# Optimization experiments

Hardware: AMD Instinct MI355X
Metric: run time of the kernel (lower is better)

## Reference

```python
import jax, jax.numpy as jnp
import numpy as np

B, H, S, D = 4, 16, 2048, 64


def setup_inputs() -> dict:
    key = jax.random.key(0)
    kq, kk, kv = jax.random.split(key, 3)
    q = jax.random.normal(kq, (B, H, S, D), dtype=jnp.float32)
    k = jax.random.normal(kk, (B, H, S, D), dtype=jnp.float32)
    v = jax.random.normal(kv, (B, H, S, D), dtype=jnp.float32)
    mask = jnp.tril(jnp.ones((S, S), dtype=jnp.bool_))  # causal: True = attend
    return {"q": q, "k": k, "v": v, "mask": mask}


def reference(q, k, v, mask):
    d_k = q.shape[-1]
    scale = 1.0 / jnp.sqrt(jnp.asarray(d_k, q.dtype))
    # scores: [B, H, S_q, S_k] -- full O(N^2) matrix, faithful to original
    score = jnp.einsum('bhqd,bhkd->bhqk', q, k) * scale
    score = jnp.where(mask, score, jnp.asarray(-jnp.inf, score.dtype))
    attn = jax.nn.softmax(score, axis=-1)
    return jnp.einsum('bhqk,bhkd->bhqd', attn, v)
```

## Files before the change

### kernel.cpp

```cpp
#include <hip/hip_runtime.h>
#include <hip/hip_bf16.h>

typedef __attribute__((ext_vector_type(8))) short short8_t;
typedef __attribute__((ext_vector_type(16))) float f32x16;
typedef __attribute__((ext_vector_type(4))) unsigned uint4_t;

constexpr int S  = 2048;
constexpr int D  = 64;
constexpr int BQ = 128;
constexpr int KV = 64;
constexpr int NQ = S / BQ;
constexpr int NT = S / KV;
constexpr int BH_C = 64;
constexpr float THR = 8.f;

static __device__ __forceinline__ unsigned packbf(float lo, float hi) {
  __hip_bfloat162 p = __float22bfloat162_rn(float2{lo, hi});
  return (unsigned)__bfloat16_as_ushort(p.x) | ((unsigned)__bfloat16_as_ushort(p.y) << 16);
}
static __device__ __forceinline__ short8_t pack8(float4 a, float4 b) {
  uint4_t u = { packbf(a.x, a.y), packbf(a.z, a.w), packbf(b.x, b.y), packbf(b.z, b.w) };
  return __builtin_bit_cast(short8_t, u);
}
static __device__ __forceinline__ float vmax16(const f32x16& a) {
  float x0 = fmaxf(a[0], a[1]),   x1 = fmaxf(a[2], a[3]);
  float x2 = fmaxf(a[4], a[5]),   x3 = fmaxf(a[6], a[7]);
  float x4 = fmaxf(a[8], a[9]),   x5 = fmaxf(a[10], a[11]);
  float x6 = fmaxf(a[12], a[13]), x7 = fmaxf(a[14], a[15]);
  x0 = fmaxf(x0, x1); x2 = fmaxf(x2, x3); x4 = fmaxf(x4, x5); x6 = fmaxf(x6, x7);
  return fmaxf(fmaxf(x0, x2), fmaxf(x4, x6));
}

static __device__ __forceinline__ void build_pfrags(const f32x16& p, int h,
                                                    short8_t& f0, short8_t& f1) {
  unsigned W0 = packbf(p[0],  p[1]),  W1 = packbf(p[2],  p[3]);
  unsigned W2 = packbf(p[4],  p[5]),  W3 = packbf(p[6],  p[7]);
  unsigned W4 = packbf(p[8],  p[9]),  W5 = packbf(p[10], p[11]);
  unsigned W6 = packbf(p[12], p[13]), W7 = packbf(p[14], p[15]);
  unsigned e0 = __shfl_xor(W0, 32), e1 = __shfl_xor(W1, 32);
  unsigned e2 = __shfl_xor(W2, 32), e3 = __shfl_xor(W3, 32);
  unsigned e4 = __shfl_xor(W4, 32), e5 = __shfl_xor(W5, 32);
  unsigned e6 = __shfl_xor(W6, 32), e7 = __shfl_xor(W7, 32);
  uint4_t u0, u1;
  if (h) { u0 = uint4_t{e2, e3, W2, W3}; u1 = uint4_t{e6, e7, W6, W7}; }
  else   { u0 = uint4_t{W0, W1, e0, e1}; u1 = uint4_t{W4, W5, e4, e5}; }
  f0 = __builtin_bit_cast(short8_t, u0);
  f1 = __builtin_bit_cast(short8_t, u1);
}

__global__ __launch_bounds__(256)
void prep_kernel(const float* __restrict__ k, const float* __restrict__ v,
                 short* __restrict__ kb, short* __restrict__ vtb)
{
  const int tile = (int)blockIdx.x;
  const int bh   = (int)blockIdx.y;
  const int tid  = (int)threadIdx.x;
  const int kv0  = tile * KV;
  const int srow = tid >> 2, sch = tid & 3;

  __shared__ float vt[KV][D + 4];

  {
    const float* kp = k + ((size_t)bh * S + kv0 + srow) * D + sch * 16;
    float4 a0 = *(const float4*)(kp);     float4 a1 = *(const float4*)(kp + 4);
    float4 a2 = *(const float4*)(kp + 8); float4 a3 = *(const float4*)(kp + 12);
    short* kd = kb + ((size_t)bh * S + kv0 + srow) * D;
    *(short8_t*)&kd[((2 * sch)     ^ (srow & 7)) * 8] = pack8(a0, a1);
    *(short8_t*)&kd[((2 * sch + 1) ^ (srow & 7)) * 8] = pack8(a2, a3);

    const float* vp = v + ((size_t)bh * S + kv0 + srow) * D + sch * 16;
    float4 b0 = *(const float4*)(vp);     float4 b1 = *(const float4*)(vp + 4);
    float4 b2 = *(const float4*)(vp + 8); float4 b3 = *(const float4*)(vp + 12);
    *(float4*)&vt[srow][sch * 16 + 0]  = b0;
    *(float4*)&vt[srow][sch * 16 + 4]  = b1;
    *(float4*)&vt[srow][sch * 16 + 8]  = b2;
    *(float4*)&vt[srow][sch * 16 + 12] = b3;
  }
  __syncthreads();
  {
    const int d = tid >> 2, q4 = tid & 3;
    float f[16];
    #pragma unroll
    for (int jj = 0; jj < 16; ++jj) f[jj] = vt[16 * q4 + jj][d];
    float4 c0 = make_float4(f[0],  f[1],  f[2],  f[3]);
    float4 c1 = make_float4(f[4],  f[5],  f[6],  f[7]);
    float4 c2 = make_float4(f[8],  f[9],  f[10], f[11]);
    float4 c3 = make_float4(f[12], f[13], f[14], f[15]);
    short* vd = vtb + (size_t)bh * S * D + (size_t)tile * KV * D + d * 64;
    *(short8_t*)&vd[((2 * q4)     ^ (d & 7)) * 8] = pack8(c0, c1);
    *(short8_t*)&vd[((2 * q4 + 1) ^ (d & 7)) * 8] = pack8(c2, c3);
  }
}

__global__ __launch_bounds__(256, 2)
void fattn8_kernel(const float* __restrict__ q, const short* __restrict__ kb,
                   const short* __restrict__ vtb, float* __restrict__ out)
{
  const int bid  = (int)blockIdx.x;
  const int qblk = NQ - 1 - (bid >> 6);
  const int bh   = bid & (BH_C - 1);
  const int tid  = (int)threadIdx.x;
  const int wave = tid >> 6;
  const int lane = tid & 63;
  const int h    = lane >> 5;
  const int ln   = lane & 31;

  const int qb = qblk * BQ;
  const int qw = qb + wave * 32;
  const int qi = qw + ln;
  const int qmax_w = qw + 31;
  const int ntseg = 2 * (qblk + 1);

  __shared__ short bufK[2][KV * D];
  __shared__ short bufV[2][KV * D];

  const short* kbase = kb  + (size_t)bh * S * D;
  const short* vbase = vtb + (size_t)bh * S * D;

  short8_t rk0, rk1, rv0, rv1;
  auto issue = [&](int t) {
    const short* gk = kbase + (size_t)t * (KV * D) + tid * 16;
    rk0 = *(const short8_t*)gk; rk1 = *(const short8_t*)(gk + 8);
    const short* gv = vbase + (size_t)t * (KV * D) + tid * 16;
    rv0 = *(const short8_t*)gv; rv1 = *(const short8_t*)(gv + 8);
  };
  issue(0);
  int cur = 0;

  const float qscale = 0.125f * 1.4426950408889634f;

  short8_t aq[4];
  {
    const float* qp = q + ((size_t)bh * S + qi) * D + 8 * h;
    #pragma unroll
    for (int ks = 0; ks < 4; ++ks) {
      float4 lo = *(const float4*)(qp + 16 * ks);
      float4 hi = *(const float4*)(qp + 16 * ks + 4);
      lo.x *= qscale; lo.y *= qscale; lo.z *= qscale; lo.w *= qscale;
      hi.x *= qscale; hi.y *= qscale; hi.z *= qscale; hi.w *= qscale;
      aq[ks] = pack8(lo, hi);
    }
  }

  f32x16 o0, o1;
  #pragma unroll
  for (int r = 0; r < 16; ++r) { o0[r] = 0.f; o1[r] = 0.f; }
  float m = -INFINITY, lsum = 0.f;

  #pragma unroll 1
  for (int i = 0; i < ntseg; ++i) {
    {
      short* dK = &bufK[cur][tid * 16];
      *(short8_t*)dK = rk0; *(short8_t*)(dK + 8) = rk1;
      short* dV = &bufV[cur][tid * 16];
      *(short8_t*)dV = rv0; *(short8_t*)(dV + 8) = rv1;
    }
    if (i + 1 < ntseg) issue(i + 1);
    __syncthreads();

    const int kv0 = i * KV;
    if (kv0 <= qmax_w) {
      const bool hi_live = (kv0 + 32 <= qmax_w);
      const short* Kc = bufK[cur];
      const short* Vc = bufV[cur];

      f32x16 st0, st1;
      #pragma unroll
      for (int r = 0; r < 16; ++r) { st0[r] = 0.f; st1[r] = 0.f; }
      #pragma unroll
      for (int ks = 0; ks < 4; ++ks) {
        short8_t kf0 = *(const short8_t*)&Kc[ln * D + (((2 * ks + h) ^ (ln & 7)) * 8)];
        st0 = __builtin_amdgcn_mfma_f32_32x32x16_bf16(kf0, aq[ks], st0, 0, 0, 0);
      }
      if (hi_live) {
        #pragma unroll
        for (int ks = 0; ks < 4; ++ks) {
          short8_t kf1 = *(const short8_t*)&Kc[(32 + ln) * D + (((2 * ks + h) ^ (ln & 7)) * 8)];
          st1 = __builtin_amdgcn_mfma_f32_32x32x16_bf16(kf1, aq[ks], st1, 0, 0, 0);
        }
      }

      if (kv0 + KV - 1 > qw) {
        #pragma unroll
        for (int r = 0; r < 16; ++r) {
          const int kvr = kv0 + (r & 3) + 8 * (r >> 2) + 4 * h;
          st0[r] = (kvr > qi) ? -INFINITY : st0[r];
          if (hi_live) st1[r] = (kvr + 32 > qi) ? -INFINITY : st1[r];
        }
      }

      float tm = hi_live ? fmaxf(vmax16(st0), vmax16(st1)) : vmax16(st0);
      tm = fmaxf(tm, __shfl_xor(tm, 32));
      if (!__all(tm <= m + THR)) {
        const float mn = fmaxf(m, tm);
        const float al = exp2f(m - mn);
        m = mn;
        lsum *= al;
        #pragma unroll
        for (int r = 0; r < 16; ++r) { o0[r] *= al; o1[r] *= al; }
      }
      float ssum = 0.f;
      #pragma unroll
      for (int r = 0; r < 16; ++r) { st0[r] = exp2f(st0[r] - m); ssum += st0[r]; }
      if (hi_live) {
        #pragma unroll
        for (int r = 0; r < 16; ++r) { st1[r] = exp2f(st1[r] - m); ssum += st1[r]; }
      }
      ssum += __shfl_xor(ssum, 32);
      lsum += ssum;

      short8_t p00, p01, p10, p11;
      build_pfrags(st0, h, p00, p01);
      if (hi_live) build_pfrags(st1, h, p10, p11);
      #pragma unroll
      for (int dt = 0; dt < 2; ++dt) {
        const int dr = 32 * dt + ln;
        f32x16 &o = dt ? o1 : o0;
        short8_t vf00 = *(const short8_t*)&Vc[dr * 64 + (((0 + h) ^ (dr & 7)) * 8)];
        short8_t vf01 = *(const short8_t*)&Vc[dr * 64 + (((2 + h) ^ (dr & 7)) * 8)];
        o = __builtin_amdgcn_mfma_f32_32x32x16_bf16(vf00, p00, o, 0, 0, 0);
        o = __builtin_amdgcn_mfma_f32_32x32x16_bf16(vf01, p01, o, 0, 0, 0);
        if (hi_live) {
          short8_t vf10 = *(const short8_t*)&Vc[dr * 64 + (((4 + h) ^ (dr & 7)) * 8)];
          short8_t vf11 = *(const short8_t*)&Vc[dr * 64 + (((6 + h) ^ (dr & 7)) * 8)];
          o = __builtin_amdgcn_mfma_f32_32x32x16_bf16(vf10, p10, o, 0, 0, 0);
          o = __builtin_amdgcn_mfma_f32_32x32x16_bf16(vf11, p11, o, 0, 0, 0);
        }
      }
    }
    cur ^= 1;
  }

  const float inv = 1.f / fmaxf(lsum, 1e-37f);
  float* op = out + ((size_t)bh * S + qi) * D;
  #pragma unroll
  for (int r = 0; r < 16; ++r) {
    const int dr = (r & 3) + 8 * (r >> 2) + 4 * h;
    op[dr]      = o0[r] * inv;
    op[32 + dr] = o1[r] * inv;
  }
}

__global__ __launch_bounds__(256, 2)
void fattn3_kernel(const float* __restrict__ q, const float* __restrict__ k,
                   const float* __restrict__ v, float* __restrict__ out)
{
  const int pair = (int)blockIdx.x;
  const int bh   = (int)blockIdx.y;
  const int tid  = (int)threadIdx.x;
  const int wave = tid >> 6;
  const int lane = tid & 63;
  const int h    = lane >> 5;
  const int ln   = lane & 31;

  __shared__ short smem[BQ * D];
  short* Ks = smem;
  short* Vs = smem + KV * D;

  const float qscale = 0.125f * 1.4426950408889634f;
  const int srow = tid >> 2;
  const int sch  = tid & 3;

  #pragma unroll 1
  for (int seg = 0; seg < 2; ++seg) {
    const int qblk = seg ? (NQ - 1 - pair) : pair;
    const int qb = qblk * BQ;
    const int qw = qb + wave * 32;
    const int qi = qw + ln;
    const int qmax_w = qw + 31;
    const int kv_end = qb + BQ;

    __syncthreads();
    {
      const int r  = tid >> 1;
      const int h2 = tid & 1;
      const float* qp = q + ((size_t)bh * S + qb + r) * D + h2 * 32;
      #pragma unroll
      for (int jq = 0; jq < 4; ++jq) {
        float4 a = *(const float4*)(qp + jq * 8);
        float4 b = *(const float4*)(qp + jq * 8 + 4);
        a.x *= qscale; a.y *= qscale; a.z *= qscale; a.w *= qscale;
        b.x *= qscale; b.y *= qscale; b.z *= qscale; b.w *= qscale;
        *(short8_t*)&smem[r * D + (((4 * h2 + jq) ^ (r & 7)) * 8)] = pack8(a, b);
      }
    }
    __syncthreads();

    short8_t aq[4];
    {
      const int R = wave * 32 + ln;
      #pragma unroll
      for (int ks = 0; ks < 4; ++ks)
        aq[ks] = *(const short8_t*)&smem[R * D + (((2 * ks + h) ^ (R & 7)) * 8)];
    }
    __syncthreads();

    f32x16 o0, o1;
    #pragma unroll
    for (int r = 0; r < 16; ++r) { o0[r] = 0.f; o1[r] = 0.f; }
    float m = -INFINITY, lsum = 0.f;

    for (int kv0 = 0; kv0 < kv_end; kv0 += KV) {
      const float* kp = k + ((size_t)bh * S + kv0 + srow) * D + sch * 16;
      const float* vp = v + ((size_t)bh * S + kv0 + srow) * D + sch * 16;
      float4 k0 = *(const float4*)(kp);     float4 k1 = *(const float4*)(kp + 4);
      float4 k2 = *(const float4*)(kp + 8); float4 k3 = *(const float4*)(kp + 12);
      float4 v0 = *(const float4*)(vp);     float4 v1 = *(const float4*)(vp + 4);
      float4 v2 = *(const float4*)(vp + 8); float4 v3 = *(const float4*)(vp + 12);

      __syncthreads();
      *(short8_t*)&Ks[srow * D + (((2 * sch)     ^ (srow & 7)) * 8)] = pack8(k0, k1);
      *(short8_t*)&Ks[srow * D + (((2 * sch + 1) ^ (srow & 7)) * 8)] = pack8(k2, k3);
      {
        float vf[16] = { v0.x,v0.y,v0.z,v0.w, v1.x,v1.y,v1.z,v1.w,
                         v2.x,v2.y,v2.z,v2.w, v3.x,v3.y,v3.z,v3.w };
        #pragma unroll
        for (int jv = 0; jv < 16; jv += 2) {
          const unsigned pw = packbf(vf[jv], vf[jv + 1]);
          const int d0 = 16 * sch + jv, d1 = d0 + 1;
          Vs[d0 * 64 + (((srow >> 3) ^ (d0 & 7)) * 8) + (srow & 7)] = (short)(pw & 0xffffu);
          Vs[d1 * 64 + (((srow >> 3) ^ (d1 & 7)) * 8) + (srow & 7)] = (short)(pw >> 16);
        }
      }
      __syncthreads();

      if (kv0 <= qmax_w) {
        const bool hi_live = (kv0 + 32 <= qmax_w);
        f32x16 st0, st1;
        #pragma unroll
        for (int r = 0; r < 16; ++r) { st0[r] = 0.f; st1[r] = 0.f; }
        #pragma unroll
        for (int ks = 0; ks < 4; ++ks) {
          short8_t kf0 = *(const short8_t*)&Ks[ln * D + (((2 * ks + h) ^ (ln & 7)) * 8)];
          st0 = __builtin_amdgcn_mfma_f32_32x32x16_bf16(kf0, aq[ks], st0, 0, 0, 0);
        }
        if (hi_live) {
          #pragma unroll
          for (int ks = 0; ks < 4; ++ks) {
            short8_t kf1 = *(const short8_t*)&Ks[(32 + ln) * D + (((2 * ks + h) ^ (ln & 7)) * 8)];
            st1 = __builtin_amdgcn_mfma_f32_32x32x16_bf16(kf1, aq[ks], st1, 0, 0, 0);
          }
        }
        if (kv0 + KV - 1 > qw) {
          #pragma unroll
          for (int r = 0; r < 16; ++r) {
            const int kvr = kv0 + (r & 3) + 8 * (r >> 2) + 4 * h;
            st0[r] = (kvr > qi) ? -INFINITY : st0[r];
            if (hi_live) st1[r] = (kvr + 32 > qi) ? -INFINITY : st1[r];
          }
        }
        float tm = hi_live ? fmaxf(vmax16(st0), vmax16(st1)) : vmax16(st0);
        tm = fmaxf(tm, __shfl_xor(tm, 32));
        if (!__all(tm <= m + THR)) {
          const float mn = fmaxf(m, tm);
          const float al = exp2f(m - mn);
          m = mn;
          lsum *= al;
          #pragma unroll
          for (int r = 0; r < 16; ++r) { o0[r] *= al; o1[r] *= al; }
        }
        float ssum = 0.f;
        #pragma unroll
        for (int r = 0; r < 16; ++r) { st0[r] = exp2f(st0[r] - m); ssum += st0[r]; }
        if (hi_live) {
          #pragma unroll
          for (int r = 0; r < 16; ++r) { st1[r] = exp2f(st1[r] - m); ssum += st1[r]; }
        }
        ssum += __shfl_xor(ssum, 32);
        lsum += ssum;

        short8_t p00, p01, p10, p11;
        build_pfrags(st0, h, p00, p01);
        if (hi_live) build_pfrags(st1, h, p10, p11);
        #pragma unroll
        for (int dt = 0; dt < 2; ++dt) {
          const int dr = 32 * dt + ln;
          f32x16 &o = dt ? o1 : o0;
          short8_t vf00 = *(const short8_t*)&Vs[dr * 64 + (((0 + h) ^ (dr & 7)) * 8)];
          short8_t vf01 = *(const short8_t*)&Vs[dr * 64 + (((2 + h) ^ (dr & 7)) * 8)];
          o = __builtin_amdgcn_mfma_f32_32x32x16_bf16(vf00, p00, o, 0, 0, 0);
          o = __builtin_amdgcn_mfma_f32_32x32x16_bf16(vf01, p01, o, 0, 0, 0);
          if (hi_live) {
            short8_t vf10 = *(const short8_t*)&Vs[dr * 64 + (((4 + h) ^ (dr & 7)) * 8)];
            short8_t vf11 = *(const short8_t*)&Vs[dr * 64 + (((6 + h) ^ (dr & 7)) * 8)];
            o = __builtin_amdgcn_mfma_f32_32x32x16_bf16(vf10, p10, o, 0, 0, 0);
            o = __builtin_amdgcn_mfma_f32_32x32x16_bf16(vf11, p11, o, 0, 0, 0);
          }
        }
      }
    }

    const float inv = 1.f / fmaxf(lsum, 1e-37f);
    float* op = out + ((size_t)bh * S + qi) * D;
    #pragma unroll
    for (int r = 0; r < 16; ++r) {
      const int dr = (r & 3) + 8 * (r >> 2) + 4 * h;
      op[dr]      = o0[r] * inv;
      op[32 + dr] = o1[r] * inv;
    }
  }
}

extern "C" void kernel_launch(void* const* d_in, const int* in_sizes, int n_in,
                              void* d_out, int out_size, void* d_ws, size_t ws_size,
                              hipStream_t stream) {
  const float* q = (const float*)d_in[0];
  const float* k = (const float*)d_in[1];
  const float* v = (const float*)d_in[2];
  float* out = (float*)d_out;
  const int BH = in_sizes[0] / (S * D);
  const size_t need = (size_t)BH * S * D * 2  * 2 ;
  if (ws_size >= need && BH == BH_C) {
    short* kbw  = (short*)d_ws;
    short* vtbw = kbw + (size_t)BH * S * D;
    prep_kernel<<<dim3(NT, BH), 256, 0, stream>>>(k, v, kbw, vtbw);
    fattn8_kernel<<<dim3(NQ * BH), 256, 0, stream>>>(q, kbw, vtbw, out);
  } else {
    fattn3_kernel<<<dim3(NQ / 2, BH), 256, 0, stream>>>(q, k, v, out);
  }
}
```

Measured before the change: 94.35 us.

## Read K/V fragments directly from global memory instead of staging through LDS

Drops the double-buffered shared-memory staging of K and V tiles along with its per-tile __syncthreads. Each wave now loads its MFMA fragments straight from the pre-swizzled global bf16 buffers and runs only its own live tile count, so waves stop waiting on the block's slowest wave. The cost is that the four waves of a block each fetch the same K/V tiles through the caches, with no software prefetch to hide global latency, so MFMA work may stall on memory.

```diff
diff --git a/kernel.cpp b/kernel.cpp
--- a/kernel.cpp
+++ b/kernel.cpp
@@ -93,7 +93,7 @@
 }
 
 __global__ __launch_bounds__(256, 2)
-void fattn8_kernel(const float* __restrict__ q, const short* __restrict__ kb,
+void fattn9_kernel(const float* __restrict__ q, const short* __restrict__ kb,
                    const short* __restrict__ vtb, float* __restrict__ out)
 {
   const int bid  = (int)blockIdx.x;
@@ -105,27 +105,13 @@
   const int h    = lane >> 5;
   const int ln   = lane & 31;
 
-  const int qb = qblk * BQ;
-  const int qw = qb + wave * 32;
+  const int qw = qblk * BQ + wave * 32;
   const int qi = qw + ln;
   const int qmax_w = qw + 31;
-  const int ntseg = 2 * (qblk + 1);
-
-  __shared__ short bufK[2][KV * D];
-  __shared__ short bufV[2][KV * D];
+  const int nlive = (qw >> 6) + 1;
 
   const short* kbase = kb  + (size_t)bh * S * D;
   const short* vbase = vtb + (size_t)bh * S * D;
-
-  short8_t rk0, rk1, rv0, rv1;
-  auto issue = [&](int t) {
-    const short* gk = kbase + (size_t)t * (KV * D) + tid * 16;
-    rk0 = *(const short8_t*)gk; rk1 = *(const short8_t*)(gk + 8);
-    const short* gv = vbase + (size_t)t * (KV * D) + tid * 16;
-    rv0 = *(const short8_t*)gv; rv1 = *(const short8_t*)(gv + 8);
-  };
-  issue(0);
-  int cur = 0;
 
   const float qscale = 0.125f * 1.4426950408889634f;
 
@@ -148,87 +134,75 @@
   float m = -INFINITY, lsum = 0.f;
 
   #pragma unroll 1
-  for (int i = 0; i < ntseg; ++i) {
-    {
-      short* dK = &bufK[cur][tid * 16];
-      *(short8_t*)dK = rk0; *(short8_t*)(dK + 8) = rk1;
-      short* dV = &bufV[cur][tid * 16];
-      *(short8_t*)dV = rv0; *(short8_t*)(dV + 8) = rv1;
-    }
-    if (i + 1 < ntseg) issue(i + 1);
-    __syncthreads();
-
+  for (int i = 0; i < nlive; ++i) {
     const int kv0 = i * KV;
-    if (kv0 <= qmax_w) {
-      const bool hi_live = (kv0 + 32 <= qmax_w);
-      const short* Kc = bufK[cur];
-      const short* Vc = bufV[cur];
-
-      f32x16 st0, st1;
-      #pragma unroll
-      for (int r = 0; r < 16; ++r) { st0[r] = 0.f; st1[r] = 0.f; }
+    const bool hi_live = (kv0 + 32 <= qmax_w);
+    const short* Kc = kbase + (size_t)i * (KV * D);
+    const short* Vc = vbase + (size_t)i * (KV * D);
+
+    f32x16 st0, st1;
+    #pragma unroll
+    for (int r = 0; r < 16; ++r) { st0[r] = 0.f; st1[r] = 0.f; }
+    #pragma unroll
+    for (int ks = 0; ks < 4; ++ks) {
+      short8_t kf0 = *(const short8_t*)&Kc[ln * D + (((2 * ks + h) ^ (ln & 7)) * 8)];
+      st0 = __builtin_amdgcn_mfma_f32_32x32x16_bf16(kf0, aq[ks], st0, 0, 0, 0);
+    }
+    if (hi_live) {
       #pragma unroll
       for (int ks = 0; ks < 4; ++ks) {
-        short8_t kf0 = *(const short8_t*)&Kc[ln * D + (((2 * ks + h) ^ (ln & 7)) * 8)];
-        st0 = __builtin_amdgcn_mfma_f32_32x32x16_bf16(kf0, aq[ks], st0, 0, 0, 0);
-      }
+        short8_t kf1 = *(const short8_t*)&Kc[(32 + ln) * D + (((2 * ks + h) ^ (ln & 7)) * 8)];
+        st1 = __builtin_amdgcn_mfma_f32_32x32x16_bf16(kf1, aq[ks], st1, 0, 0, 0);
+      }
+    }
+
+    if (kv0 + KV - 1 > qw) {
+      #pragma unroll
+      for (int r = 0; r < 16; ++r) {
+        const int kvr = kv0 + (r & 3) + 8 * (r >> 2) + 4 * h;
+        st0[r] = (kvr > qi) ? -INFINITY : st0[r];
+        if (hi_live) st1[r] = (kvr + 32 > qi) ? -INFINITY : st1[r];
+      }
+    }
+
+    float tm = hi_live ? fmaxf(vmax16(st0), vmax16(st1)) : vmax16(st0);
+    tm = fmaxf(tm, __shfl_xor(tm, 32));
+    if (!__all(tm <= m + THR)) {
+      const float mn = fmaxf(m, tm);
+      const float al = exp2f(m - mn);
+      m = mn;
+      lsum *= al;
+      #pragma unroll
+      for (int r = 0; r < 16; ++r) { o0[r] *= al; o1[r] *= al; }
+    }
+    float ssum = 0.f;
+    #pragma unroll
+    for (int r = 0; r < 16; ++r) { st0[r] = exp2f(st0[r] - m); ssum += st0[r]; }
+    if (hi_live) {
+      #pragma unroll
+      for (int r = 0; r < 16; ++r) { st1[r] = exp2f(st1[r] - m); ssum += st1[r]; }
+    }
+    ssum += __shfl_xor(ssum, 32);
+    lsum += ssum;
+
+    short8_t p00, p01, p10, p11;
+    build_pfrags(st0, h, p00, p01);
+    if (hi_live) build_pfrags(st1, h, p10, p11);
+    #pragma unroll
+    for (int dt = 0; dt < 2; ++dt) {
+      const int dr = 32 * dt + ln;
+      f32x16 &o = dt ? o1 : o0;
+      short8_t vf00 = *(const short8_t*)&Vc[dr * 64 + (((0 + h) ^ (dr & 7)) * 8)];
+      short8_t vf01 = *(const short8_t*)&Vc[dr * 64 + (((2 + h) ^ (dr & 7)) * 8)];
+      o = __builtin_amdgcn_mfma_f32_32x32x16_bf16(vf00, p00, o, 0, 0, 0);
+      o = __builtin_amdgcn_mfma_f32_32x32x16_bf16(vf01, p01, o, 0, 0, 0);
       if (hi_live) {
-        #pragma unroll
-        for (int ks = 0; ks < 4; ++ks) {
-          short8_t kf1 = *(const short8_t*)&Kc[(32 + ln) * D + (((2 * ks + h) ^ (ln & 7)) * 8)];
-          st1 = __builtin_amdgcn_mfma_f32_32x32x16_bf16(kf1, aq[ks], st1, 0, 0, 0);
-        }
-      }
-
-      if (kv0 + KV - 1 > qw) {
-        #pragma unroll
-        for (int r = 0; r < 16; ++r) {
-          const int kvr = kv0 + (r & 3) + 8 * (r >> 2) + 4 * h;
-          st0[r] = (kvr > qi) ? -INFINITY : st0[r];
-          if (hi_live) st1[r] = (kvr + 32 > qi) ? -INFINITY : st1[r];
-        }
-      }
-
-      float tm = hi_live ? fmaxf(vmax16(st0), vmax16(st1)) : vmax16(st0);
-      tm = fmaxf(tm, __shfl_xor(tm, 32));
-      if (!__all(tm <= m + THR)) {
-        const float mn = fmaxf(m, tm);
-        const float al = exp2f(m - mn);
-        m = mn;
-        lsum *= al;
-        #pragma unroll
-        for (int r = 0; r < 16; ++r) { o0[r] *= al; o1[r] *= al; }
-      }
-      float ssum = 0.f;
-      #pragma unroll
-      for (int r = 0; r < 16; ++r) { st0[r] = exp2f(st0[r] - m); ssum += st0[r]; }
-      if (hi_live) {
-        #pragma unroll
-        for (int r = 0; r < 16; ++r) { st1[r] = exp2f(st1[r] - m); ssum += st1[r]; }
-      }
-      ssum += __shfl_xor(ssum, 32);
-      lsum += ssum;
-
-      short8_t p00, p01, p10, p11;
-      build_pfrags(st0, h, p00, p01);
-      if (hi_live) build_pfrags(st1, h, p10, p11);
-      #pragma unroll
-      for (int dt = 0; dt < 2; ++dt) {
-        const int dr = 32 * dt + ln;
-        f32x16 &o = dt ? o1 : o0;
-        short8_t vf00 = *(const short8_t*)&Vc[dr * 64 + (((0 + h) ^ (dr & 7)) * 8)];
-        short8_t vf01 = *(const short8_t*)&Vc[dr * 64 + (((2 + h) ^ (dr & 7)) * 8)];
-        o = __builtin_amdgcn_mfma_f32_32x32x16_bf16(vf00, p00, o, 0, 0, 0);
-        o = __builtin_amdgcn_mfma_f32_32x32x16_bf16(vf01, p01, o, 0, 0, 0);
-        if (hi_live) {
-          short8_t vf10 = *(const short8_t*)&Vc[dr * 64 + (((4 + h) ^ (dr & 7)) * 8)];
-          short8_t vf11 = *(const short8_t*)&Vc[dr * 64 + (((6 + h) ^ (dr & 7)) * 8)];
-          o = __builtin_amdgcn_mfma_f32_32x32x16_bf16(vf10, p10, o, 0, 0, 0);
-          o = __builtin_amdgcn_mfma_f32_32x32x16_bf16(vf11, p11, o, 0, 0, 0);
-        }
-      }
-    }
-    cur ^= 1;
+        short8_t vf10 = *(const short8_t*)&Vc[dr * 64 + (((4 + h) ^ (dr & 7)) * 8)];
+        short8_t vf11 = *(const short8_t*)&Vc[dr * 64 + (((6 + h) ^ (dr & 7)) * 8)];
+        o = __builtin_amdgcn_mfma_f32_32x32x16_bf16(vf10, p10, o, 0, 0, 0);
+        o = __builtin_amdgcn_mfma_f32_32x32x16_bf16(vf11, p11, o, 0, 0, 0);
+      }
+    }
   }
 
   const float inv = 1.f / fmaxf(lsum, 1e-37f);
@@ -414,7 +388,7 @@
     short* kbw  = (short*)d_ws;
     short* vtbw = kbw + (size_t)BH * S * D;
     prep_kernel<<<dim3(NT, BH), 256, 0, stream>>>(k, v, kbw, vtbw);
-    fattn8_kernel<<<dim3(NQ * BH), 256, 0, stream>>>(q, kbw, vtbw, out);
+    fattn9_kernel<<<dim3(NQ * BH), 256, 0, stream>>>(q, kbw, vtbw, out);
   } else {
     fattn3_kernel<<<dim3(NQ / 2, BH), 256, 0, stream>>>(q, k, v, out);
   }
```

Result: slower. 108.9 us (+15.5%).

## Interleave causal q-block scheduling order and split softmax row-sum accumulators

Applied to the files above, without the earlier changes.

Block-to-q-tile mapping changes from strictly descending q-block order to an interleaved order. Groups of heavy and light causal tiles alternate (15..12, 0..3, 11..8, 4..7), so the tail of the grid is better balanced across CUs. The exp/sum loop uses four independent partial sums instead of one serial accumulator, to shorten the dependency chain. The new order may reduce load balance if the hardware dispatch order differs from the assumed one. The changed summation order alters float rounding slightly.

```diff
diff --git a/kernel.cpp b/kernel.cpp
--- a/kernel.cpp
+++ b/kernel.cpp
@@ -93,11 +93,17 @@
 }
 
 __global__ __launch_bounds__(256, 2)
-void fattn8_kernel(const float* __restrict__ q, const short* __restrict__ kb,
-                   const short* __restrict__ vtb, float* __restrict__ out)
+void fattn12_kernel(const float* __restrict__ q, const short* __restrict__ kb,
+                    const short* __restrict__ vtb, float* __restrict__ out)
 {
-  const int bid  = (int)blockIdx.x;
-  const int qblk = NQ - 1 - (bid >> 6);
+  const int bid = (int)blockIdx.x;
+  const int r4 = bid >> 8;
+  const int g  = (bid >> 6) & 3;
+  int qblk;
+  if      (r4 == 0) qblk = 15 - g;
+  else if (r4 == 1) qblk = g;
+  else if (r4 == 2) qblk = 11 - g;
+  else              qblk = 4 + g;
   const int bh   = bid & (BH_C - 1);
   const int tid  = (int)threadIdx.x;
   const int wave = tid >> 6;
@@ -105,8 +111,7 @@
   const int h    = lane >> 5;
   const int ln   = lane & 31;
 
-  const int qb = qblk * BQ;
-  const int qw = qb + wave * 32;
+  const int qw = qblk * BQ + wave * 32;
   const int qi = qw + ln;
   const int qmax_w = qw + 31;
   const int ntseg = 2 * (qblk + 1);
@@ -199,13 +204,24 @@
         #pragma unroll
         for (int r = 0; r < 16; ++r) { o0[r] *= al; o1[r] *= al; }
       }
-      float ssum = 0.f;
-      #pragma unroll
-      for (int r = 0; r < 16; ++r) { st0[r] = exp2f(st0[r] - m); ssum += st0[r]; }
+      float s0 = 0.f, s1 = 0.f, s2 = 0.f, s3 = 0.f;
+      #pragma unroll
+      for (int r = 0; r < 16; r += 4) {
+        st0[r]     = exp2f(st0[r]     - m); s0 += st0[r];
+        st0[r + 1] = exp2f(st0[r + 1] - m); s1 += st0[r + 1];
+        st0[r + 2] = exp2f(st0[r + 2] - m); s2 += st0[r + 2];
+        st0[r + 3] = exp2f(st0[r + 3] - m); s3 += st0[r + 3];
+      }
       if (hi_live) {
         #pragma unroll
-        for (int r = 0; r < 16; ++r) { st1[r] = exp2f(st1[r] - m); ssum += st1[r]; }
-      }
+        for (int r = 0; r < 16; r += 4) {
+          st1[r]     = exp2f(st1[r]     - m); s0 += st1[r];
+          st1[r + 1] = exp2f(st1[r + 1] - m); s1 += st1[r + 1];
+          st1[r + 2] = exp2f(st1[r + 2] - m); s2 += st1[r + 2];
+          st1[r + 3] = exp2f(st1[r + 3] - m); s3 += st1[r + 3];
+        }
+      }
+      float ssum = (s0 + s1) + (s2 + s3);
       ssum += __shfl_xor(ssum, 32);
       lsum += ssum;
 
@@ -414,7 +430,7 @@
     short* kbw  = (short*)d_ws;
     short* vtbw = kbw + (size_t)BH * S * D;
     prep_kernel<<<dim3(NT, BH), 256, 0, stream>>>(k, v, kbw, vtbw);
-    fattn8_kernel<<<dim3(NQ * BH), 256, 0, stream>>>(q, kbw, vtbw, out);
+    fattn12_kernel<<<dim3(NQ * BH), 256, 0, stream>>>(q, kbw, vtbw, out);
   } else {
     fattn3_kernel<<<dim3(NQ / 2, BH), 256, 0, stream>>>(q, k, v, out);
   }
```

After: 95.79 us. No clear change (+1.5%).
